# Kernel tuning notes

Measured on AMD Instinct MI355X. Metric: run time of the kernel, lower is better.

Reference implementation:

```python
import jax, jax.numpy as jnp
import numpy as np

N, E, D = 100000, 1600000, 128  # nodes, edges, hidden=in=out channels


def setup_inputs() -> dict:
    key = jax.random.key(0)
    ks = jax.random.split(key, 10)
    s = 1.0 / np.sqrt(D)
    return {
        "x": jax.random.normal(ks[0], (N, D), dtype=jnp.float32),
        "edge_index": jax.random.randint(ks[1], (2, E), 0, N, dtype=jnp.int64),
        # lin_in: in_ch -> hidden
        "W_in": jax.random.uniform(ks[2], (D, D), jnp.float32, -s, s),
        "b_in": jnp.zeros((D,), jnp.float32),
        # GatedGraphConv per-step message weight (x @ W_msg, no transpose)
        "W_msg": jax.random.uniform(ks[3], (D, D), jnp.float32, -s, s),
        # GRUCell params, gate order (r, z, n)
        "W_ih": jax.random.uniform(ks[4], (3 * D, D), jnp.float32, -s, s),
        "b_ih": jax.random.uniform(ks[5], (3 * D,), jnp.float32, -s, s),
        "W_hh": jax.random.uniform(ks[6], (3 * D, D), jnp.float32, -s, s),
        "b_hh": jax.random.uniform(ks[7], (3 * D,), jnp.float32, -s, s),
        # lin_out: hidden -> out_ch
        "W_out": jax.random.uniform(ks[8], (D, D), jnp.float32, -s, s),
        "b_out": jnp.zeros((D,), jnp.float32),
    }


def reference(x, edge_index, W_in, b_in, W_msg, W_ih, b_ih, W_hh, b_hh, W_out, b_out):
    n_nodes = x.shape[0]
    src, dst = edge_index[0], edge_index[1]
    # input projection: [N, D]
    h = x @ W_in.T + b_in
    # GatedGraphConv single step: m = h @ W_msg, then scatter-add src -> dst
    m = h @ W_msg
    agg = jax.ops.segment_sum(m[src], dst, num_segments=n_nodes)  # [N, D]
    # GRUCell update: h' = GRU(input=agg, hidden=h)
    gi = agg @ W_ih.T + b_ih  # [N, 3D]
    gh = h @ W_hh.T + b_hh    # [N, 3D]
    i_r, i_z, i_n = jnp.split(gi, 3, axis=-1)
    h_r, h_z, h_n = jnp.split(gh, 3, axis=-1)
    r = jax.nn.sigmoid(i_r + h_r)
    z = jax.nn.sigmoid(i_z + h_z)
    n = jnp.tanh(i_n + r * h_n)
    h_new = (1.0 - z) * n + z * h
    # output projection
    return h_new @ W_out.T + b_out
```

## Files before the change

### kernel.cpp

```cpp
#include <hip/hip_runtime.h>
#include <math.h>

#define DD 128
#define RING 32
#define MAXB 400
#define CAPSH 13
#define WCAP 248
#define NBIN_BLOCKS 256

using bf16x8 = __attribute__((ext_vector_type(8))) short;
using f32x4  = __attribute__((ext_vector_type(4))) float;

__device__ inline unsigned short f2bf(float f) {
    unsigned int u = __float_as_uint(f);
    unsigned int r = (u + 0x7fffu + ((u >> 16) & 1u)) >> 16;
    return (unsigned short)r;
}
__device__ inline float bf2f(unsigned short h) {
    return __uint_as_float(((unsigned int)h) << 16);
}

#define MFMA16(a, b, c) __builtin_amdgcn_mfma_f32_16x16x32_bf16((a), (b), (c), 0, 0, 0)

__device__ inline void stageW(float4* lds, const unsigned short* W, int tid) {
    const float4* src = reinterpret_cast<const float4*>(W);
#pragma unroll
    for (int it = 0; it < 8; ++it) {
        int i = tid + it * 256;
        int n = i >> 4, ch = i & 15;
        lds[n * 16 + (ch ^ (n & 15))] = src[i];
    }
}

__device__ inline bf16x8 fragL(const float4* lds, int lane, int s, int r) {
    float4 v = lds[r * 16 + (((s << 2) + (lane >> 4)) ^ (r & 15))];
    return __builtin_bit_cast(bf16x8, v);
}

__device__ inline bf16x8 fragG(const unsigned short* A, long row, int koff) {
    float4 v = *reinterpret_cast<const float4*>(A + row * DD + koff);
    return __builtin_bit_cast(bf16x8, v);
}

__device__ inline bf16x8 fragGF(const float* A, long row, int koff) {
    const float4* p = reinterpret_cast<const float4*>(A + row * DD + koff);
    float4 a = p[0], b = p[1];
    bf16x8 r;
    r[0] = f2bf(a.x); r[1] = f2bf(a.y); r[2] = f2bf(a.z); r[3] = f2bf(a.w);
    r[4] = f2bf(b.x); r[5] = f2bf(b.y); r[6] = f2bf(b.z); r[7] = f2bf(b.w);
    return r;
}

__global__ __launch_bounds__(256) void wconv(
    const float* __restrict__ W_in, const float* __restrict__ W_msg,
    const float* __restrict__ W_ih, const float* __restrict__ W_hh,
    const float* __restrict__ W_out, unsigned short* __restrict__ wb,
    int* __restrict__ gcur)
{
    int i = blockIdx.x * 256 + threadIdx.x;
    if (i < 16384) wb[i] = f2bf(W_in[i]);
    else if (i < 32768) {
        int j = i - 16384; int n = j >> 7, k = j & 127;
        wb[i] = f2bf(W_msg[k * DD + n]);
    }
    else if (i < 81920)  wb[i] = f2bf(W_ih[i - 32768]);
    else if (i < 131072) wb[i] = f2bf(W_hh[i - 81920]);
    else if (i < 147456) wb[i] = f2bf(W_out[i - 131072]);
    else if (i < 148480) gcur[i - 147456] = 0;
}

__device__ void bin_edges_body(char* smem, int bid,
    const int* __restrict__ ei, int E, int nbc,
    unsigned int* __restrict__ bucket, int* __restrict__ gcur,
    int* __restrict__ govf, unsigned long long* __restrict__ ovf)
{
    unsigned int (*ring)[RING] = (unsigned int (*)[RING])smem;
    int* lres = (int*)(smem + MAXB * RING * 4);
    int* lfl  = lres + MAXB;
    const int tid = threadIdx.x;
    for (int b = tid; b < MAXB; b += 256) { lres[b] = 0; lfl[b] = 0; }
    __syncthreads();

    const int nt = (E + 255) >> 8;
    for (int t = bid; t < nt; t += NBIN_BLOCKS) {
        const int e = (t << 8) + tid;
        if (e < E) {
            const int d = ei[E + e];
            const int s = ei[e];
            const int b = d >> 8;
            const unsigned int ent = ((unsigned int)s << 8) | (unsigned int)(d & 255);
            const int pos = atomicAdd(&lres[b], 1);
            if (pos - lfl[b] >= RING) {
                const int op = atomicAdd(govf, 1);
                ovf[op] = ((unsigned long long)(unsigned int)s << 32) | (unsigned int)d;
            } else {
                ring[b][pos & (RING - 1)] = ent;
            }
        }
        __syncthreads();
        for (int bb = tid; bb < nbc; bb += 256) {
            const int res = lres[bb];
            const int fl = lfl[bb];
            const int lim = fl + RING;
            const bool drain = res > lim;
            const int hi = drain ? lim : res;
            const int avail = hi - fl;
            const int nf = drain ? avail : (avail & ~15);
            if (nf > 0) {
                const int gp = atomicAdd(&gcur[bb], nf);
                unsigned int* dst = bucket + ((size_t)bb << CAPSH) + gp;
                for (int k = 0; k < nf; ++k) dst[k] = ring[bb][(fl + k) & (RING - 1)];
            }
            lfl[bb] = drain ? res : fl + nf;
        }
        __syncthreads();
    }
    for (int bb = tid; bb < nbc; bb += 256) {
        const int res = lres[bb];
        const int fl = lfl[bb];
        const int avail = res - fl;
        if (avail > 0) {
            const int gp = atomicAdd(&gcur[bb], avail);
            unsigned int* dst = bucket + ((size_t)bb << CAPSH) + gp;
            for (int k = 0; k < avail; ++k) dst[k] = ring[bb][(fl + k) & (RING - 1)];
        }
    }
}

__device__ void k12_body(char* smem, int bid,
    const float* __restrict__ x, const unsigned short* __restrict__ Wi,
    const unsigned short* __restrict__ Wm, const float* __restrict__ b_in,
    unsigned short* __restrict__ h_bf, unsigned short* __restrict__ m_bf, int M)
{
    float4* WA = (float4*)smem;
    float4* WB = (float4*)(smem + 32768);
    const int tid = threadIdx.x;
    const int lane = tid & 63;
    const int w = tid >> 6;
    const int c15 = lane & 15;
    const int hi = lane >> 4;
    const long base = (long)bid * 64;
    long arow = base + w * 16 + c15;
    if (arow >= M) arow = M - 1;

    stageW(WA, Wi, tid);
    stageW(WB, Wm, tid);
    __syncthreads();

    f32x4 acc[8];
#pragma unroll
    for (int ct = 0; ct < 8; ++ct) acc[ct] = (f32x4){0.f, 0.f, 0.f, 0.f};
#pragma unroll 1
    for (int s = 0; s < 4; ++s) {
        bf16x8 a = fragGF(x, arow, s * 32 + 8 * hi);
#pragma unroll
        for (int ct = 0; ct < 8; ++ct)
            acc[ct] = MFMA16(a, fragL(WA, lane, s, ct * 16 + c15), acc[ct]);
    }
    __syncthreads();

    unsigned short* Hu = reinterpret_cast<unsigned short*>(WA);
#pragma unroll
    for (int ct = 0; ct < 8; ++ct)
#pragma unroll
        for (int j = 0; j < 4; ++j) {
            int rloc = w * 16 + 4 * hi + j;
            long r = base + rloc;
            int c = ct * 16 + c15;
            float v = acc[ct][j] + b_in[c];
            unsigned short hv = f2bf(v);
            Hu[rloc * DD + ((c >> 3) ^ (rloc & 15)) * 8 + (c & 7)] = hv;
            if (r < M) h_bf[r * DD + c] = hv;
        }
    __syncthreads();

#pragma unroll
    for (int ct = 0; ct < 8; ++ct) acc[ct] = (f32x4){0.f, 0.f, 0.f, 0.f};
#pragma unroll 1
    for (int s = 0; s < 4; ++s) {
        bf16x8 a = fragL(WA, lane, s, w * 16 + c15);
#pragma unroll
        for (int ct = 0; ct < 8; ++ct)
            acc[ct] = MFMA16(a, fragL(WB, lane, s, ct * 16 + c15), acc[ct]);
    }
#pragma unroll
    for (int ct = 0; ct < 8; ++ct)
#pragma unroll
        for (int j = 0; j < 4; ++j) {
            long r = base + w * 16 + 4 * hi + j;
            if (r < M) m_bf[r * DD + ct * 16 + c15] = f2bf(acc[ct][j]);
        }
}

__global__ __launch_bounds__(256) void front(
    const int* __restrict__ ei, int E, int nbc,
    unsigned int* __restrict__ bucket, int* __restrict__ gcur,
    int* __restrict__ govf, unsigned long long* __restrict__ ovf,
    const float* __restrict__ x, const unsigned short* __restrict__ Wi,
    const unsigned short* __restrict__ Wm, const float* __restrict__ b_in,
    unsigned short* __restrict__ h_bf, unsigned short* __restrict__ m_bf, int M)
{
    __shared__ char smem[65536];
    if (blockIdx.x < NBIN_BLOCKS)
        bin_edges_body(smem, blockIdx.x, ei, E, nbc, bucket, gcur, govf, ovf);
    else
        k12_body(smem, blockIdx.x - NBIN_BLOCKS, x, Wi, Wm, b_in, h_bf, m_bf, M);
}

__global__ __launch_bounds__(256, 8) void bin_reduce(
    const unsigned short* __restrict__ m,
    const unsigned int* __restrict__ bucket, const int* __restrict__ gcur,
    const int* __restrict__ govf, const unsigned long long* __restrict__ ovf,
    unsigned short* __restrict__ agg, int N)
{
    __shared__ float acc[32 * DD];
    __shared__ unsigned int wlist[4][WCAP];
    const int tid = threadIdx.x, lane = tid & 63, wv = tid >> 6;
    const int cb = blockIdx.x >> 3, q = blockIdx.x & 7;

    {
        float4* a4 = (float4*)acc;
        const float4 z = {0.f, 0.f, 0.f, 0.f};
        for (int i = tid; i < 32 * DD / 4; i += 256) a4[i] = z;
    }

    int cnt = gcur[cb];
    if (cnt > (1 << CAPSH)) cnt = 1 << CAPSH;
    const unsigned int* bb = bucket + ((size_t)cb << CAPSH);

    int nw = 0;
    bool ovfw = false;
    for (int c0 = 0; c0 < cnt; c0 += 64) {
        const int idx = c0 + lane;
        const unsigned int ent = (idx < cnt) ? bb[idx] : 0u;
        const int dl = ent & 255;
        const bool mine = (idx < cnt) && ((dl >> 5) == q) && ((dl & 3) == wv);
        const unsigned long long mask = __ballot(mine);
        if (mine) {
            const int p = __popcll(mask & ((1ull << lane) - 1));
            const int pos = nw + p;
            if (pos < WCAP) wlist[wv][pos] = ent;
            else ovfw = true;
        }
        nw += __popcll(mask);
    }
    const int nmy = (nw < WCAP) ? nw : WCAP;
    __syncthreads();

    int i = 0;
    for (; i + 8 <= nmy; i += 8) {
        unsigned int e[8], mv[8];
#pragma unroll
        for (int j = 0; j < 8; ++j) e[j] = wlist[wv][i + j];
#pragma unroll
        for (int j = 0; j < 8; ++j)
            mv[j] = *(const unsigned int*)(m + ((size_t)(e[j] >> 8)) * DD + lane * 2);
#pragma unroll
        for (int j = 0; j < 8; ++j) {
            float2* p = (float2*)&acc[(e[j] & 31) * DD + lane * 2];
            float2 v = *p;
            v.x += bf2f((unsigned short)(mv[j] & 0xffff));
            v.y += bf2f((unsigned short)(mv[j] >> 16));
            *p = v;
        }
    }
    for (; i < nmy; ++i) {
        const unsigned int e0 = wlist[wv][i];
        const unsigned int mv0 = *(const unsigned int*)(m + ((size_t)(e0 >> 8)) * DD + lane * 2);
        float2* p = (float2*)&acc[(e0 & 31) * DD + lane * 2];
        float2 v = *p;
        v.x += bf2f((unsigned short)(mv0 & 0xffff));
        v.y += bf2f((unsigned short)(mv0 >> 16));
        *p = v;
    }

    if (__ballot(ovfw)) {
        if (ovfw) {
            int cum = 0;
            for (int c0 = 0; c0 < cnt; c0 += 64) {
                const int idx = c0 + lane;
                const unsigned int ent = (idx < cnt) ? bb[idx] : 0u;
                const int dl = ent & 255;
                const bool mine = (idx < cnt) && ((dl >> 5) == q) && ((dl & 3) == wv);
                unsigned long long mask = __ballot(mine);
                unsigned long long mm = mask;
                int k = 0;
                while (mm) {
                    const int l = __builtin_ctzll(mm); mm &= mm - 1;
                    if (cum + k >= WCAP) {
                        const unsigned int ee = __shfl(ent, l);
                        const unsigned int mvv = *(const unsigned int*)(m + ((size_t)(ee >> 8)) * DD + lane * 2);
                        float2* p = (float2*)&acc[(ee & 31) * DD + lane * 2];
                        float2 v = *p;
                        v.x += bf2f((unsigned short)(mvv & 0xffff));
                        v.y += bf2f((unsigned short)(mvv >> 16));
                        *p = v;
                    }
                    ++k;
                }
                cum += __popcll(mask);
            }
        }
    }

    const int novf = *govf;
    for (int i2 = 0; i2 < novf; ++i2) {
        const unsigned long long v = ovf[i2];
        const int d = (int)(v & 0xffffffffu);
        if ((d >> 8) != cb) continue;
        const int dl = d & 255;
        if ((dl >> 5) != q || (dl & 3) != wv) continue;
        const int src = (int)(v >> 32);
        const unsigned int mv = *(const unsigned int*)(m + (size_t)src * DD + lane * 2);
        float2* p = (float2*)&acc[(dl & 31) * DD + lane * 2];
        float2 vv = *p;
        vv.x += bf2f((unsigned short)(mv & 0xffff));
        vv.y += bf2f((unsigned short)(mv >> 16));
        *p = vv;
    }
    __syncthreads();

    const long rbase = (long)cb * 256 + (long)q * 32;
    for (int r = wv; r < 32; r += 4) {
        const long rg = rbase + r;
        if (rg < N) {
            const float a0 = acc[r * DD + lane * 2];
            const float a1 = acc[r * DD + lane * 2 + 1];
            const unsigned int pk = ((unsigned int)f2bf(a1) << 16) | f2bf(a0);
            *(unsigned int*)(agg + rg * DD + lane * 2) = pk;
        }
    }
}

__global__ __launch_bounds__(256) void gru8(
    const unsigned short* __restrict__ agg, const unsigned short* __restrict__ hbf,
    const unsigned short* __restrict__ Wih, const unsigned short* __restrict__ Whh,
    const unsigned short* __restrict__ Wo,
    const float* __restrict__ b_ih, const float* __restrict__ b_hh,
    const float* __restrict__ b_out, float* __restrict__ out, int M)
{
    __shared__ float4 WA[2048];
    __shared__ float4 WB[2048];
    const int tid = threadIdx.x;
    const int lane = tid & 63;
    const int w = tid >> 6;
    const int c15 = lane & 15;
    const int hi = lane >> 4;
    const long base = (long)blockIdx.x * 64;
    long arow = base + w * 16 + c15;
    if (arow >= M) arow = M - 1;

    f32x4 acc[8];
    float rg[32], zg[32];

    stageW(WA, Wih, tid);
    stageW(WB, Whh, tid);
    __syncthreads();
#pragma unroll
    for (int ct = 0; ct < 8; ++ct) acc[ct] = (f32x4){0.f, 0.f, 0.f, 0.f};
#pragma unroll 1
    for (int s = 0; s < 4; ++s) {
        bf16x8 ai = fragG(agg, arow, s * 32 + 8 * hi);
        bf16x8 ah = fragG(hbf, arow, s * 32 + 8 * hi);
#pragma unroll
        for (int ct = 0; ct < 8; ++ct) {
            acc[ct] = MFMA16(ai, fragL(WA, lane, s, ct * 16 + c15), acc[ct]);
            acc[ct] = MFMA16(ah, fragL(WB, lane, s, ct * 16 + c15), acc[ct]);
        }
    }
#pragma unroll
    for (int ct = 0; ct < 8; ++ct)
#pragma unroll
        for (int j = 0; j < 4; ++j) {
            int c = ct * 16 + c15;
            float v = acc[ct][j] + b_ih[c] + b_hh[c];
            rg[ct * 4 + j] = 1.f / (1.f + __expf(-v));
        }
    __syncthreads();

    stageW(WA, Wih + 16384, tid);
    stageW(WB, Whh + 16384, tid);
    __syncthreads();
#pragma unroll
    for (int ct = 0; ct < 8; ++ct) acc[ct] = (f32x4){0.f, 0.f, 0.f, 0.f};
#pragma unroll 1
    for (int s = 0; s < 4; ++s) {
        bf16x8 ai = fragG(agg, arow, s * 32 + 8 * hi);
        bf16x8 ah = fragG(hbf, arow, s * 32 + 8 * hi);
#pragma unroll
        for (int ct = 0; ct < 8; ++ct) {
            acc[ct] = MFMA16(ai, fragL(WA, lane, s, ct * 16 + c15), acc[ct]);
            acc[ct] = MFMA16(ah, fragL(WB, lane, s, ct * 16 + c15), acc[ct]);
        }
    }
#pragma unroll
    for (int ct = 0; ct < 8; ++ct)
#pragma unroll
        for (int j = 0; j < 4; ++j) {
            int c = ct * 16 + c15;
            float v = acc[ct][j] + b_ih[DD + c] + b_hh[DD + c];
            zg[ct * 4 + j] = 1.f / (1.f + __expf(-v));
        }
    __syncthreads();

    stageW(WA, Wih + 32768, tid);
    stageW(WB, Whh + 32768, tid);
    __syncthreads();
    f32x4 acch[8];
#pragma unroll
    for (int ct = 0; ct < 8; ++ct) {
        acc[ct] = (f32x4){0.f, 0.f, 0.f, 0.f};
        acch[ct] = (f32x4){0.f, 0.f, 0.f, 0.f};
    }
#pragma unroll 1
    for (int s = 0; s < 4; ++s) {
        bf16x8 ai = fragG(agg, arow, s * 32 + 8 * hi);
        bf16x8 ah = fragG(hbf, arow, s * 32 + 8 * hi);
#pragma unroll
        for (int ct = 0; ct < 8; ++ct) {
            acc[ct]  = MFMA16(ai, fragL(WA, lane, s, ct * 16 + c15), acc[ct]);
            acch[ct] = MFMA16(ah, fragL(WB, lane, s, ct * 16 + c15), acch[ct]);
        }
    }
    __syncthreads();

    unsigned short* Hu = reinterpret_cast<unsigned short*>(WA);
#pragma unroll
    for (int ct = 0; ct < 8; ++ct)
#pragma unroll
        for (int j = 0; j < 4; ++j) {
            int c = ct * 16 + c15;
            int rloc = w * 16 + 4 * hi + j;
            long r = base + rloc;
            long rr = (r < M) ? r : (M - 1);
            float inb = acc[ct][j] + b_ih[2 * DD + c];
            float hnb = acch[ct][j] + b_hh[2 * DD + c];
            float n = tanhf(inb + rg[ct * 4 + j] * hnb);
            float hv = bf2f(hbf[rr * DD + c]);
            float z = zg[ct * 4 + j];
            float hnew = (1.f - z) * n + z * hv;
            Hu[rloc * DD + ((c >> 3) ^ (rloc & 15)) * 8 + (c & 7)] = f2bf(hnew);
        }
    stageW(WB, Wo, tid);
    __syncthreads();

#pragma unroll
    for (int ct = 0; ct < 8; ++ct) acc[ct] = (f32x4){0.f, 0.f, 0.f, 0.f};
#pragma unroll 1
    for (int s = 0; s < 4; ++s) {
        bf16x8 a = fragL(WA, lane, s, w * 16 + c15);
#pragma unroll
        for (int ct = 0; ct < 8; ++ct)
            acc[ct] = MFMA16(a, fragL(WB, lane, s, ct * 16 + c15), acc[ct]);
    }
#pragma unroll
    for (int ct = 0; ct < 8; ++ct)
#pragma unroll
        for (int j = 0; j < 4; ++j) {
            long r = base + w * 16 + 4 * hi + j;
            if (r < M) out[r * DD + ct * 16 + c15] = acc[ct][j] + b_out[ct * 16 + c15];
        }
}

extern "C" void kernel_launch(void* const* d_in, const int* in_sizes, int n_in,
                              void* d_out, int out_size, void* d_ws, size_t ws_size,
                              hipStream_t stream) {
    const float* x     = (const float*)d_in[0];
    const int*   ei    = (const int*)d_in[1];
    const float* W_in  = (const float*)d_in[2];
    const float* b_in  = (const float*)d_in[3];
    const float* W_msg = (const float*)d_in[4];
    const float* W_ih  = (const float*)d_in[5];
    const float* b_ih  = (const float*)d_in[6];
    const float* W_hh  = (const float*)d_in[7];
    const float* b_hh  = (const float*)d_in[8];
    const float* W_out = (const float*)d_in[9];
    const float* b_out = (const float*)d_in[10];

    const int N = in_sizes[0] / DD;
    const int E = in_sizes[1] / 2;
    float* out = (float*)d_out;

    const size_t slotE = (size_t)N * DD;
    unsigned short* wb     = (unsigned short*)d_ws;
    unsigned short* h_bf   = (unsigned short*)((char*)d_ws + (1 << 19));
    unsigned short* m_bf   = h_bf + slotE;
    unsigned short* agg_bf = m_bf + slotE;

    const int nbc = (N + 255) >> 8;
    unsigned int* bucket = (unsigned int*)d_out;
    int* gcur = (int*)((char*)d_out + (16u << 20));
    int* govf = gcur + 512;
    unsigned long long* ovf = (unsigned long long*)(gcur + 1024);

    dim3 blk(256);
    const int gblocks = (N + 63) / 64;

    wconv<<<(148480 + 255) / 256, blk, 0, stream>>>(W_in, W_msg, W_ih, W_hh, W_out, wb, gcur);
    front<<<NBIN_BLOCKS + gblocks, blk, 0, stream>>>(ei, E, nbc, bucket, gcur, govf, ovf,
                                                     x, wb, wb + 16384, b_in, h_bf, m_bf, N);
    bin_reduce<<<nbc * 8, blk, 0, stream>>>(m_bf, bucket, gcur, govf, ovf, agg_bf, N);
    gru8<<<gblocks, blk, 0, stream>>>(agg_bf, h_bf, wb + 32768, wb + 81920, wb + 131072,
                                      b_ih, b_hh, b_out, out, N);
}
```

Measured before the change: 262.8 us.

## Pre-swizzle weights, cut GRU LDS footprint, cache A fragments, fast activations

The weight conversion kernel now writes bf16 weights already in the XOR-swizzled LDS layout, so staging into shared memory becomes a plain linear copy. The GRU kernel keeps the agg and h row fragments in registers, uses a single shared weight buffer plus a small H tile instead of two full weight buffers, and asks for three blocks per CU. The aim is less LDS per block and higher occupancy, at the cost of more barriers and serialized weight reloads. The r and z gates are stored packed as bf16, sigmoid and tanh use fast reciprocal and exp forms that lose some precision, and the scatter loop is rewritten with 32-bit loads.

```diff
diff --git a/kernel.cpp b/kernel.cpp
--- a/kernel.cpp
+++ b/kernel.cpp
@@ -19,17 +19,21 @@
 __device__ inline float bf2f(unsigned short h) {
     return __uint_as_float(((unsigned int)h) << 16);
 }
+__device__ inline float fsig(float v) {
+    return __builtin_amdgcn_rcpf(1.f + __expf(-v));
+}
+__device__ inline float ftanh(float v) {
+    float x = fminf(15.f, fmaxf(-15.f, v));
+    float t = __expf(2.f * x);
+    return (t - 1.f) * __builtin_amdgcn_rcpf(t + 1.f);
+}
 
 #define MFMA16(a, b, c) __builtin_amdgcn_mfma_f32_16x16x32_bf16((a), (b), (c), 0, 0, 0)
 
-__device__ inline void stageW(float4* lds, const unsigned short* W, int tid) {
-    const float4* src = reinterpret_cast<const float4*>(W);
-#pragma unroll
-    for (int it = 0; it < 8; ++it) {
-        int i = tid + it * 256;
-        int n = i >> 4, ch = i & 15;
-        lds[n * 16 + (ch ^ (n & 15))] = src[i];
-    }
+__device__ inline void copyW(float4* dst, const unsigned short* W, int tid) {
+    const float4* s4 = reinterpret_cast<const float4*>(W);
+#pragma unroll
+    for (int it = 0; it < 8; ++it) dst[tid + it * 256] = s4[tid + it * 256];
 }
 
 __device__ inline bf16x8 fragL(const float4* lds, int lane, int s, int r) {
@@ -58,15 +62,20 @@
     int* __restrict__ gcur)
 {
     int i = blockIdx.x * 256 + threadIdx.x;
-    if (i < 16384) wb[i] = f2bf(W_in[i]);
-    else if (i < 32768) {
-        int j = i - 16384; int n = j >> 7, k = j & 127;
-        wb[i] = f2bf(W_msg[k * DD + n]);
-    }
-    else if (i < 81920)  wb[i] = f2bf(W_ih[i - 32768]);
-    else if (i < 131072) wb[i] = f2bf(W_hh[i - 81920]);
-    else if (i < 147456) wb[i] = f2bf(W_out[i - 131072]);
-    else if (i < 148480) gcur[i - 147456] = 0;
+    if (i < 147456) {
+        int slice = i >> 14;
+        int r = i & 16383;
+        int n = r >> 7, k = r & 127;
+        float v;
+        if (slice == 0)      v = W_in[r];
+        else if (slice == 1) v = W_msg[k * DD + n];
+        else if (slice <= 4) v = W_ih[(slice - 2) * 16384 + r];
+        else if (slice <= 7) v = W_hh[(slice - 5) * 16384 + r];
+        else                 v = W_out[r];
+        wb[(i & ~16383) + n * 128 + (((k >> 3) ^ (n & 15)) << 3) + (k & 7)] = f2bf(v);
+    } else if (i < 148480) {
+        gcur[i - 147456] = 0;
+    }
 }
 
 __device__ void bin_edges_body(char* smem, int bid,
@@ -143,8 +152,8 @@
     long arow = base + w * 16 + c15;
     if (arow >= M) arow = M - 1;
 
-    stageW(WA, Wi, tid);
-    stageW(WB, Wm, tid);
+    copyW(WA, Wi, tid);
+    copyW(WB, Wm, tid);
     __syncthreads();
 
     f32x4 acc[8];
@@ -169,7 +178,7 @@
             int c = ct * 16 + c15;
             float v = acc[ct][j] + b_in[c];
             unsigned short hv = f2bf(v);
-            Hu[rloc * DD + ((c >> 3) ^ (rloc & 15)) * 8 + (c & 7)] = hv;
+            Hu[rloc * DD + (((c >> 3) ^ (rloc & 15)) << 3) + (c & 7)] = hv;
             if (r < M) h_bf[r * DD + c] = hv;
         }
     __syncthreads();
@@ -200,7 +209,8 @@
     const unsigned short* __restrict__ Wm, const float* __restrict__ b_in,
     unsigned short* __restrict__ h_bf, unsigned short* __restrict__ m_bf, int M)
 {
-    __shared__ char smem[65536];
+    __shared__ float4 smem4[4096];
+    char* smem = (char*)smem4;
     if (blockIdx.x < NBIN_BLOCKS)
         bin_edges_body(smem, blockIdx.x, ei, E, nbc, bucket, gcur, govf, ovf);
     else
@@ -247,32 +257,38 @@
     const int nmy = (nw < WCAP) ? nw : WCAP;
     __syncthreads();
 
+    const unsigned int* mu = (const unsigned int*)m;
     int i = 0;
     for (; i + 8 <= nmy; i += 8) {
-        unsigned int e[8], mv[8];
-#pragma unroll
-        for (int j = 0; j < 8; ++j) e[j] = wlist[wv][i + j];
-#pragma unroll
-        for (int j = 0; j < 8; ++j)
-            mv[j] = *(const unsigned int*)(m + ((size_t)(e[j] >> 8)) * DD + lane * 2);
-#pragma unroll
-        for (int j = 0; j < 8; ++j) {
-            float2* p = (float2*)&acc[(e[j] & 31) * DD + lane * 2];
-            float2 v = *p;
-            v.x += bf2f((unsigned short)(mv[j] & 0xffff));
-            v.y += bf2f((unsigned short)(mv[j] >> 16));
-            *p = v;
-        }
+        const unsigned int e0 = wlist[wv][i + 0], e1 = wlist[wv][i + 1];
+        const unsigned int e2 = wlist[wv][i + 2], e3 = wlist[wv][i + 3];
+        const unsigned int e4 = wlist[wv][i + 4], e5 = wlist[wv][i + 5];
+        const unsigned int e6 = wlist[wv][i + 6], e7 = wlist[wv][i + 7];
+        const unsigned int v0 = mu[(size_t)(e0 >> 8) * 64 + lane];
+        const unsigned int v1 = mu[(size_t)(e1 >> 8) * 64 + lane];
+        const unsigned int v2 = mu[(size_t)(e2 >> 8) * 64 + lane];
+        const unsigned int v3 = mu[(size_t)(e3 >> 8) * 64 + lane];
+        const unsigned int v4 = mu[(size_t)(e4 >> 8) * 64 + lane];
+        const unsigned int v5 = mu[(size_t)(e5 >> 8) * 64 + lane];
+        const unsigned int v6 = mu[(size_t)(e6 >> 8) * 64 + lane];
+        const unsigned int v7 = mu[(size_t)(e7 >> 8) * 64 + lane];
+        float2* p;
+        float2 a;
+#define RMW(EE, VV) \
+        p = (float2*)&acc[((EE) & 31) * DD + lane * 2]; a = *p; \
+        a.x += bf2f((unsigned short)((VV) & 0xffff)); \
+        a.y += bf2f((unsigned short)((VV) >> 16)); *p = a;
+        RMW(e0, v0) RMW(e1, v1) RMW(e2, v2) RMW(e3, v3)
+        RMW(e4, v4) RMW(e5, v5) RMW(e6, v6) RMW(e7, v7)
     }
     for (; i < nmy; ++i) {
         const unsigned int e0 = wlist[wv][i];
-        const unsigned int mv0 = *(const unsigned int*)(m + ((size_t)(e0 >> 8)) * DD + lane * 2);
-        float2* p = (float2*)&acc[(e0 & 31) * DD + lane * 2];
-        float2 v = *p;
-        v.x += bf2f((unsigned short)(mv0 & 0xffff));
-        v.y += bf2f((unsigned short)(mv0 >> 16));
-        *p = v;
-    }
+        const unsigned int v0 = mu[(size_t)(e0 >> 8) * 64 + lane];
+        float2* p;
+        float2 a;
+        RMW(e0, v0)
+    }
+#undef RMW
 
     if (__ballot(ovfw)) {
         if (ovfw) {
@@ -289,12 +305,12 @@
                     const int l = __builtin_ctzll(mm); mm &= mm - 1;
                     if (cum + k >= WCAP) {
                         const unsigned int ee = __shfl(ent, l);
-                        const unsigned int mvv = *(const unsigned int*)(m + ((size_t)(ee >> 8)) * DD + lane * 2);
+                        const unsigned int vv = mu[(size_t)(ee >> 8) * 64 + lane];
                         float2* p = (float2*)&acc[(ee & 31) * DD + lane * 2];
-                        float2 v = *p;
-                        v.x += bf2f((unsigned short)(mvv & 0xffff));
-                        v.y += bf2f((unsigned short)(mvv >> 16));
-                        *p = v;
+                        float2 a = *p;
+                        a.x += bf2f((unsigned short)(vv & 0xffff));
+                        a.y += bf2f((unsigned short)(vv >> 16));
+                        *p = a;
                     }
                     ++k;
                 }
@@ -311,12 +327,12 @@
         const int dl = d & 255;
         if ((dl >> 5) != q || (dl & 3) != wv) continue;
         const int src = (int)(v >> 32);
-        const unsigned int mv = *(const unsigned int*)(m + (size_t)src * DD + lane * 2);
+        const unsigned int vv = mu[(size_t)src * 64 + lane];
         float2* p = (float2*)&acc[(dl & 31) * DD + lane * 2];
-        float2 vv = *p;
-        vv.x += bf2f((unsigned short)(mv & 0xffff));
-        vv.y += bf2f((unsigned short)(mv >> 16));
-        *p = vv;
+        float2 a = *p;
+        a.x += bf2f((unsigned short)(vv & 0xffff));
+        a.y += bf2f((unsigned short)(vv >> 16));
+        *p = a;
     }
     __syncthreads();
 
@@ -332,15 +348,15 @@
     }
 }
 
-__global__ __launch_bounds__(256) void gru8(
+__global__ __launch_bounds__(256, 3) void gru8(
     const unsigned short* __restrict__ agg, const unsigned short* __restrict__ hbf,
     const unsigned short* __restrict__ Wih, const unsigned short* __restrict__ Whh,
     const unsigned short* __restrict__ Wo,
     const float* __restrict__ b_ih, const float* __restrict__ b_hh,
     const float* __restrict__ b_out, float* __restrict__ out, int M)
 {
-    __shared__ float4 WA[2048];
-    __shared__ float4 WB[2048];
+    __shared__ float4 Wbuf[2048];
+    __shared__ float4 Htile[1024];
     const int tid = threadIdx.x;
     const int lane = tid & 63;
     const int w = tid >> 6;
@@ -350,108 +366,122 @@
     long arow = base + w * 16 + c15;
     if (arow >= M) arow = M - 1;
 
-    f32x4 acc[8];
-    float rg[32], zg[32];
-
-    stageW(WA, Wih, tid);
-    stageW(WB, Whh, tid);
+    bf16x8 ai[4], ah[4];
+#pragma unroll
+    for (int s = 0; s < 4; ++s) {
+        ai[s] = fragG(agg, arow, s * 32 + 8 * hi);
+        ah[s] = fragG(hbf, arow, s * 32 + 8 * hi);
+    }
+
+    f32x4 acc[8], acch[8];
+    unsigned int rgp[16], zgp[16];
+
+    copyW(Wbuf, Wih, tid);
     __syncthreads();
 #pragma unroll
     for (int ct = 0; ct < 8; ++ct) acc[ct] = (f32x4){0.f, 0.f, 0.f, 0.f};
-#pragma unroll 1
+#pragma unroll
+    for (int s = 0; s < 4; ++s)
+#pragma unroll
+        for (int ct = 0; ct < 8; ++ct)
+            acc[ct] = MFMA16(ai[s], fragL(Wbuf, lane, s, ct * 16 + c15), acc[ct]);
+    __syncthreads();
+    copyW(Wbuf, Whh, tid);
+    __syncthreads();
+#pragma unroll
+    for (int s = 0; s < 4; ++s)
+#pragma unroll
+        for (int ct = 0; ct < 8; ++ct)
+            acc[ct] = MFMA16(ah[s], fragL(Wbuf, lane, s, ct * 16 + c15), acc[ct]);
+#pragma unroll
+    for (int ct = 0; ct < 8; ++ct) {
+        const int c = ct * 16 + c15;
+        const float b = b_ih[c] + b_hh[c];
+        const float v0 = fsig(acc[ct][0] + b), v1 = fsig(acc[ct][1] + b);
+        const float v2 = fsig(acc[ct][2] + b), v3 = fsig(acc[ct][3] + b);
+        rgp[ct * 2 + 0] = ((unsigned int)f2bf(v1) << 16) | f2bf(v0);
+        rgp[ct * 2 + 1] = ((unsigned int)f2bf(v3) << 16) | f2bf(v2);
+    }
+    __syncthreads();
+
+    copyW(Wbuf, Wih + 16384, tid);
+    __syncthreads();
+#pragma unroll
+    for (int ct = 0; ct < 8; ++ct) acc[ct] = (f32x4){0.f, 0.f, 0.f, 0.f};
+#pragma unroll
+    for (int s = 0; s < 4; ++s)
+#pragma unroll
+        for (int ct = 0; ct < 8; ++ct)
+            acc[ct] = MFMA16(ai[s], fragL(Wbuf, lane, s, ct * 16 + c15), acc[ct]);
+    __syncthreads();
+    copyW(Wbuf, Whh + 16384, tid);
+    __syncthreads();
+#pragma unroll
+    for (int s = 0; s < 4; ++s)
+#pragma unroll
+        for (int ct = 0; ct < 8; ++ct)
+            acc[ct] = MFMA16(ah[s], fragL(Wbuf, lane, s, ct * 16 + c15), acc[ct]);
+#pragma unroll
+    for (int ct = 0; ct < 8; ++ct) {
+        const int c = ct * 16 + c15;
+        const float b = b_ih[DD + c] + b_hh[DD + c];
+        const float v0 = fsig(acc[ct][0] + b), v1 = fsig(acc[ct][1] + b);
+        const float v2 = fsig(acc[ct][2] + b), v3 = fsig(acc[ct][3] + b);
+        zgp[ct * 2 + 0] = ((unsigned int)f2bf(v1) << 16) | f2bf(v0);
+        zgp[ct * 2 + 1] = ((unsigned int)f2bf(v3) << 16) | f2bf(v2);
+    }
+    __syncthreads();
+
+    copyW(Wbuf, Wih + 32768, tid);
+    __syncthreads();
+#pragma unroll
+    for (int ct = 0; ct < 8; ++ct) acc[ct] = (f32x4){0.f, 0.f, 0.f, 0.f};
+#pragma unroll
+    for (int s = 0; s < 4; ++s)
+#pragma unroll
+        for (int ct = 0; ct < 8; ++ct)
+            acc[ct] = MFMA16(ai[s], fragL(Wbuf, lane, s, ct * 16 + c15), acc[ct]);
+    __syncthreads();
+    copyW(Wbuf, Whh + 32768, tid);
+    __syncthreads();
+#pragma unroll
+    for (int ct = 0; ct < 8; ++ct) acch[ct] = (f32x4){0.f, 0.f, 0.f, 0.f};
+#pragma unroll
+    for (int s = 0; s < 4; ++s)
+#pragma unroll
+        for (int ct = 0; ct < 8; ++ct)
+            acch[ct] = MFMA16(ah[s], fragL(Wbuf, lane, s, ct * 16 + c15), acch[ct]);
+
+    unsigned short* Hu = reinterpret_cast<unsigned short*>(Htile);
+#pragma unroll
+    for (int ct = 0; ct < 8; ++ct) {
+        const int c = ct * 16 + c15;
+        const float bi = b_ih[2 * DD + c], bh = b_hh[2 * DD + c];
+#pragma unroll
+        for (int j = 0; j < 4; ++j) {
+            const int rloc = w * 16 + 4 * hi + j;
+            long rr = base + rloc;
+            if (rr >= M) rr = M - 1;
+            const float r = bf2f((unsigned short)(rgp[ct * 2 + (j >> 1)] >> ((j & 1) * 16)));
+            const float z = bf2f((unsigned short)(zgp[ct * 2 + (j >> 1)] >> ((j & 1) * 16)));
+            const float n = ftanh(acc[ct][j] + bi + r * (acch[ct][j] + bh));
+            const float hv = bf2f(hbf[rr * DD + c]);
+            const float hnew = (1.f - z) * n + z * hv;
+            Hu[rloc * DD + (((c >> 3) ^ (rloc & 15)) << 3) + (c & 7)] = f2bf(hnew);
+        }
+    }
+    __syncthreads();
+    copyW(Wbuf, Wo, tid);
+    __syncthreads();
+
+#pragma unroll
+    for (int ct = 0; ct < 8; ++ct) acc[ct] = (f32x4){0.f, 0.f, 0.f, 0.f};
+#pragma unroll
     for (int s = 0; s < 4; ++s) {
-        bf16x8 ai = fragG(agg, arow, s * 32 + 8 * hi);
-        bf16x8 ah = fragG(hbf, arow, s * 32 + 8 * hi);
-#pragma unroll
-        for (int ct = 0; ct < 8; ++ct) {
-            acc[ct] = MFMA16(ai, fragL(WA, lane, s, ct * 16 + c15), acc[ct]);
-            acc[ct] = MFMA16(ah, fragL(WB, lane, s, ct * 16 + c15), acc[ct]);
-        }
-    }
-#pragma unroll
-    for (int ct = 0; ct < 8; ++ct)
-#pragma unroll
-        for (int j = 0; j < 4; ++j) {
-            int c = ct * 16 + c15;
-            float v = acc[ct][j] + b_ih[c] + b_hh[c];
-            rg[ct * 4 + j] = 1.f / (1.f + __expf(-v));
-        }
-    __syncthreads();
-
-    stageW(WA, Wih + 16384, tid);
-    stageW(WB, Whh + 16384, tid);
-    __syncthreads();
-#pragma unroll
-    for (int ct = 0; ct < 8; ++ct) acc[ct] = (f32x4){0.f, 0.f, 0.f, 0.f};
-#pragma unroll 1
-    for (int s = 0; s < 4; ++s) {
-        bf16x8 ai = fragG(agg, arow, s * 32 + 8 * hi);
-        bf16x8 ah = fragG(hbf, arow, s * 32 + 8 * hi);
-#pragma unroll
-        for (int ct = 0; ct < 8; ++ct) {
-            acc[ct] = MFMA16(ai, fragL(WA, lane, s, ct * 16 + c15), acc[ct]);
-            acc[ct] = MFMA16(ah, fragL(WB, lane, s, ct * 16 + c15), acc[ct]);
-        }
-    }
-#pragma unroll
-    for (int ct = 0; ct < 8; ++ct)
-#pragma unroll
-        for (int j = 0; j < 4; ++j) {
-            int c = ct * 16 + c15;
-            float v = acc[ct][j] + b_ih[DD + c] + b_hh[DD + c];
-            zg[ct * 4 + j] = 1.f / (1.f + __expf(-v));
-        }
-    __syncthreads();
-
-    stageW(WA, Wih + 32768, tid);
-    stageW(WB, Whh + 32768, tid);
-    __syncthreads();
-    f32x4 acch[8];
-#pragma unroll
-    for (int ct = 0; ct < 8; ++ct) {
-        acc[ct] = (f32x4){0.f, 0.f, 0.f, 0.f};
-        acch[ct] = (f32x4){0.f, 0.f, 0.f, 0.f};
-    }
-#pragma unroll 1
-    for (int s = 0; s < 4; ++s) {
-        bf16x8 ai = fragG(agg, arow, s * 32 + 8 * hi);
-        bf16x8 ah = fragG(hbf, arow, s * 32 + 8 * hi);
-#pragma unroll
-        for (int ct = 0; ct < 8; ++ct) {
-            acc[ct]  = MFMA16(ai, fragL(WA, lane, s, ct * 16 + c15), acc[ct]);
-            acch[ct] = MFMA16(ah, fragL(WB, lane, s, ct * 16 + c15), acch[ct]);
-        }
-    }
-    __syncthreads();
-
-    unsigned short* Hu = reinterpret_cast<unsigned short*>(WA);
-#pragma unroll
-    for (int ct = 0; ct < 8; ++ct)
-#pragma unroll
-        for (int j = 0; j < 4; ++j) {
-            int c = ct * 16 + c15;
-            int rloc = w * 16 + 4 * hi + j;
-            long r = base + rloc;
-            long rr = (r < M) ? r : (M - 1);
-            float inb = acc[ct][j] + b_ih[2 * DD + c];
-            float hnb = acch[ct][j] + b_hh[2 * DD + c];
-            float n = tanhf(inb + rg[ct * 4 + j] * hnb);
-            float hv = bf2f(hbf[rr * DD + c]);
-            float z = zg[ct * 4 + j];
-            float hnew = (1.f - z) * n + z * hv;
-            Hu[rloc * DD + ((c >> 3) ^ (rloc & 15)) * 8 + (c & 7)] = f2bf(hnew);
-        }
-    stageW(WB, Wo, tid);
-    __syncthreads();
-
-#pragma unroll
-    for (int ct = 0; ct < 8; ++ct) acc[ct] = (f32x4){0.f, 0.f, 0.f, 0.f};
-#pragma unroll 1
-    for (int s = 0; s < 4; ++s) {
-        bf16x8 a = fragL(WA, lane, s, w * 16 + c15);
-#pragma unroll
-        for (int ct = 0; ct < 8; ++ct)
-            acc[ct] = MFMA16(a, fragL(WB, lane, s, ct * 16 + c15), acc[ct]);
+        bf16x8 a = fragL(Htile, lane, s, w * 16 + c15);
+#pragma unroll
+        for (int ct = 0; ct < 8; ++ct)
+            acc[ct] = MFMA16(a, fragL(Wbuf, lane, s, ct * 16 + c15), acc[ct]);
     }
 #pragma unroll
     for (int ct = 0; ct < 8; ++ct)
```

Result: slower. 288.4 us (+9.7%).
